# Kernel tuning notes

Measured on AMD Instinct MI355X. Metric: run time of the kernel, lower is better.

## Reference

```python
import jax, jax.numpy as jnp
import numpy as np


def setup_inputs() -> dict:
    key = jax.random.key(0)
    kq, kk, kv = jax.random.split(key, 3)
    B, H, S, D = 2, 16, 2048, 64
    Q = jax.random.normal(kq, (B, H, S, D), dtype=jnp.float32)
    K = jax.random.normal(kk, (B, H, S, D), dtype=jnp.float32)
    V = jax.random.normal(kv, (B, H, S, D), dtype=jnp.float32)
    # causal mask: 1 = keep, 0 = masked (masked_fill on mask == 0)
    mask = jnp.tril(jnp.ones((S, S), dtype=bool))[None, None, :, :]
    return {"V": V, "Q": Q, "K": K, "Fk": D, "mask": mask}


def reference(V, Q, K, Fk, mask):
    scale = 1.0 / jnp.sqrt(jnp.asarray(Fk, dtype=jnp.float32))
    # [B,H,S,S] scores
    C = jnp.einsum("bhqd,bhkd->bhqk", Q, K) * scale
    C = jnp.where(mask, C, jnp.asarray(-1e9, dtype=C.dtype))
    C = jax.nn.softmax(C, axis=-1)
    return jnp.einsum("bhqk,bhkd->bhqd", C, V)
```

## Files before the change

### kernel.cpp

```cpp
#include <hip/hip_runtime.h>
#include <hip/hip_bf16.h>

typedef __bf16 bf16x8 __attribute__((ext_vector_type(8)));
typedef __bf16 bf16x4 __attribute__((ext_vector_type(4)));
typedef __bf16 bf16x2 __attribute__((ext_vector_type(2)));
typedef float f32x4 __attribute__((ext_vector_type(4)));
typedef float f32x16 __attribute__((ext_vector_type(16)));

#define S_LEN 2048
#define D_DIM 64
#define NQT   32

static __device__ __forceinline__ unsigned pk2(float a, float b) {
  bf16x2 t; t[0] = (__bf16)a; t[1] = (__bf16)b;
  return __builtin_bit_cast(unsigned, t);
}

__global__ __launch_bounds__(256) void preprocess_kernel(
    const float* __restrict__ Kg, const float* __restrict__ Vg,
    unsigned char* __restrict__ Kb, unsigned char* __restrict__ Vt) {
  __shared__ float buf[2048];
  const int tid  = threadIdx.x;
  const int tile = blockIdx.x;
  const float* kg = Kg + (long)tile * 2048;
  const float* vg = Vg + (long)tile * 2048;
  unsigned char* kb = Kb + (long)tile * 4096;
  unsigned char* vt = Vt + (long)tile * 4096;

  const int l = tid & 63, f = tid >> 6, h = l >> 5;

  {
    const float* kr = kg + (l & 31) * 64 + f * 16 + h * 8;
    float4 a = *reinterpret_cast<const float4*>(kr);
    float4 b = *reinterpret_cast<const float4*>(kr + 4);
    bf16x8 t;
    t[0]=(__bf16)a.x; t[1]=(__bf16)a.y; t[2]=(__bf16)a.z; t[3]=(__bf16)a.w;
    t[4]=(__bf16)b.x; t[5]=(__bf16)b.y; t[6]=(__bf16)b.z; t[7]=(__bf16)b.w;
    *reinterpret_cast<bf16x8*>(kb + tid * 16) = t;
  }
  #pragma unroll
  for (int i = 0; i < 2; ++i) {
    int idx = tid + 256 * i;
    *reinterpret_cast<float4*>(buf + idx * 4) =
        *reinterpret_cast<const float4*>(vg + idx * 4);
  }
  __syncthreads();
  {
    int dt = f >> 1, ks = f & 1;
    int d  = dt * 32 + (l & 31);
    int k0 = ks * 16 + h * 8;
    bf16x8 t;
    #pragma unroll
    for (int j = 0; j < 8; ++j) t[j] = (__bf16)buf[(k0 + j) * 64 + d];
    *reinterpret_cast<bf16x8*>(vt + tid * 16) = t;
  }
}

__global__ __launch_bounds__(128, 4) void attn_fwd_w32s(
    const float* __restrict__ Qg, const unsigned char* __restrict__ Kb,
    const unsigned char* __restrict__ Vt, float* __restrict__ Og) {
  __shared__ float o_sm[2][32][68];
  __shared__ float m_sm[2][32];
  __shared__ float l_sm[2][32];

  const int tid  = threadIdx.x;
  const int lane = tid & 63;
  const int w    = tid >> 6;
  const int qc   = lane & 31;
  const int h    = lane >> 5;

  const int lb = blockIdx.x;
  const int e  = lb & 7;
  const int s  = lb >> 3;
  const int bh = e + 8 * (s >> 6);
  const int qg = 63 - (s & 63);
  const long base = (long)bh * (S_LEN * D_DIM);
  const int q0 = qg * 32;
  const int NT = qg + 1;

  bf16x8 qf[4];
  {
    const float qsc = 0.125f * 1.44269504f;
    const float* qp = Qg + base + (long)(q0 + qc) * D_DIM + h * 8;
    #pragma unroll
    for (int t = 0; t < 4; ++t) {
      float4 f0 = *reinterpret_cast<const float4*>(qp + t * 16);
      float4 f1 = *reinterpret_cast<const float4*>(qp + t * 16 + 4);
      bf16x8 q;
      q[0]=(__bf16)(f0.x*qsc); q[1]=(__bf16)(f0.y*qsc);
      q[2]=(__bf16)(f0.z*qsc); q[3]=(__bf16)(f0.w*qsc);
      q[4]=(__bf16)(f1.x*qsc); q[5]=(__bf16)(f1.y*qsc);
      q[6]=(__bf16)(f1.z*qsc); q[7]=(__bf16)(f1.w*qsc);
      qf[t] = q;
    }
  }

  f32x16 po0, po1;
  #pragma unroll
  for (int r = 0; r < 16; ++r) { po0[r] = 0.f; po1[r] = 0.f; }
  float m_run = -1e30f, l_run = 0.f;

  const unsigned char* kb_bh = Kb + (long)bh * 64 * 4096 + lane * 16;
  const unsigned char* vt_bh = Vt + (long)bh * 64 * 4096 + lane * 16;

  bf16x8 kfr[4], vfr[4];
  auto ldK = [&](int kt) {
    const unsigned char* p = kb_bh + (long)kt * 4096;
    #pragma unroll
    for (int t = 0; t < 4; ++t)
      kfr[t] = *reinterpret_cast<const bf16x8*>(p + t * 1024);
  };
  auto ldV = [&](int kt) {
    const unsigned char* p = vt_bh + (long)kt * 4096;
    #pragma unroll
    for (int t = 0; t < 4; ++t)
      vfr[t] = *reinterpret_cast<const bf16x8*>(p + t * 1024);
  };

  ldK(w);
  ldV(w);

  for (int kt = w; kt < NT; kt += 2) {
    const bool more = (kt + 2 < NT);

    f32x16 sa;
    #pragma unroll
    for (int r = 0; r < 16; ++r) sa[r] = 0.f;
    __builtin_amdgcn_s_setprio(1);
    #pragma unroll
    for (int t = 0; t < 4; ++t)
      sa = __builtin_amdgcn_mfma_f32_32x32x16_bf16(kfr[t], qf[t], sa, 0, 0, 0);
    __builtin_amdgcn_s_setprio(0);

    if (more) ldK(kt + 2);

    if (kt == NT - 1) {
      #pragma unroll
      for (int r = 0; r < 16; ++r)
        if (((r & 3) + 8 * (r >> 2) + 4 * h) > qc) sa[r] = -1e30f;
    }

    float rmax;
    {
      float a0 = fmaxf(fmaxf(sa[0], sa[1]),  fmaxf(sa[2], sa[3]));
      float a1 = fmaxf(fmaxf(sa[4], sa[5]),  fmaxf(sa[6], sa[7]));
      float a2 = fmaxf(fmaxf(sa[8], sa[9]),  fmaxf(sa[10], sa[11]));
      float a3 = fmaxf(fmaxf(sa[12], sa[13]), fmaxf(sa[14], sa[15]));
      rmax = fmaxf(fmaxf(a0, a1), fmaxf(a2, a3));
      rmax = fmaxf(rmax, __shfl_xor(rmax, 32));
    }

    if (__any(rmax > m_run + 8.0f)) {
      float mn    = fmaxf(m_run, rmax);
      float alpha = exp2f(m_run - mn);
      m_run = mn;
      l_run *= alpha;
      #pragma unroll
      for (int r = 0; r < 16; ++r) {
        float ar = __shfl(alpha, (r & 3) + 8 * (r >> 2) + 4 * h);
        po0[r] *= ar;
        po1[r] *= ar;
      }
    }

    #pragma unroll
    for (int r = 0; r < 16; ++r) sa[r] = exp2f(sa[r] - m_run);
    {
      float s0 = (sa[0] + sa[1]) + (sa[2] + sa[3]);
      float s1 = (sa[4] + sa[5]) + (sa[6] + sa[7]);
      float s2 = (sa[8] + sa[9]) + (sa[10] + sa[11]);
      float s3 = (sa[12] + sa[13]) + (sa[14] + sa[15]);
      float rs = (s0 + s1) + (s2 + s3);
      l_run += rs + __shfl_xor(rs, 32);
    }

    bf16x8 pa0, pa1;
    {
      unsigned k0 = pk2(sa[0], sa[1]),   k1 = pk2(sa[2], sa[3]);
      unsigned k2 = pk2(sa[4], sa[5]),   k3 = pk2(sa[6], sa[7]);
      unsigned k4 = pk2(sa[8], sa[9]),   k5 = pk2(sa[10], sa[11]);
      unsigned k6 = pk2(sa[12], sa[13]), k7 = pk2(sa[14], sa[15]);
      unsigned x02 = h ? k0 : k2, x13 = h ? k1 : k3;
      unsigned x46 = h ? k4 : k6, x57 = h ? k5 : k7;
      unsigned p02 = (unsigned)__shfl_xor((int)x02, 32);
      unsigned p13 = (unsigned)__shfl_xor((int)x13, 32);
      unsigned p46 = (unsigned)__shfl_xor((int)x46, 32);
      unsigned p57 = (unsigned)__shfl_xor((int)x57, 32);
      union { unsigned u[4]; bf16x8 v; } a, b;
      a.u[0] = h ? p02 : k0;  a.u[1] = h ? p13 : k1;
      a.u[2] = h ? k2 : p02;  a.u[3] = h ? k3 : p13;
      b.u[0] = h ? p46 : k4;  b.u[1] = h ? p57 : k5;
      b.u[2] = h ? k6 : p46;  b.u[3] = h ? k7 : p57;
      pa0 = a.v;
      pa1 = b.v;
    }

    __builtin_amdgcn_s_setprio(1);
    po0 = __builtin_amdgcn_mfma_f32_32x32x16_bf16(pa0, vfr[0], po0, 0, 0, 0);
    po0 = __builtin_amdgcn_mfma_f32_32x32x16_bf16(pa1, vfr[1], po0, 0, 0, 0);
    po1 = __builtin_amdgcn_mfma_f32_32x32x16_bf16(pa0, vfr[2], po1, 0, 0, 0);
    po1 = __builtin_amdgcn_mfma_f32_32x32x16_bf16(pa1, vfr[3], po1, 0, 0, 0);
    __builtin_amdgcn_s_setprio(0);

    if (more) ldV(kt + 2);
  }

  #pragma unroll
  for (int r = 0; r < 16; ++r) {
    int crow = (r & 3) + 8 * (r >> 2) + 4 * h;
    o_sm[w][crow][qc]      = po0[r];
    o_sm[w][crow][qc + 32] = po1[r];
  }
  if (h == 0) { m_sm[w][qc] = m_run; l_sm[w][qc] = l_run; }
  __syncthreads();

  {
    const int q  = tid >> 2;
    const int d0 = (tid & 3) * 16;
    float m0 = m_sm[0][q], m1 = m_sm[1][q];
    float M  = fmaxf(m0, m1);
    float a0 = exp2f(m0 - M), a1 = exp2f(m1 - M);
    float inv = 1.0f / (a0 * l_sm[0][q] + a1 * l_sm[1][q]);
    const float* r0 = &o_sm[0][q][d0];
    const float* r1 = &o_sm[1][q][d0];
    float* og = Og + base + (long)(q0 + q) * D_DIM + d0;
    #pragma unroll
    for (int i = 0; i < 4; ++i) {
      float4 x0 = *reinterpret_cast<const float4*>(r0 + 4 * i);
      float4 x1 = *reinterpret_cast<const float4*>(r1 + 4 * i);
      float4 o;
      o.x = (a0 * x0.x + a1 * x1.x) * inv;
      o.y = (a0 * x0.y + a1 * x1.y) * inv;
      o.z = (a0 * x0.z + a1 * x1.z) * inv;
      o.w = (a0 * x0.w + a1 * x1.w) * inv;
      *reinterpret_cast<float4*>(og + 4 * i) = o;
    }
  }
}

__global__ __launch_bounds__(256) void attn_fwd_fallback(
    const float* __restrict__ Vg, const float* __restrict__ Qg,
    const float* __restrict__ Kg, float* __restrict__ Og) {
  __shared__ __align__(16) unsigned char k_lds[64 * 128];
  __shared__ __align__(16) unsigned char vt_lds[64 * 128];
  __shared__ __align__(16) unsigned char p_lds[4][16 * 128];

  const int tid  = threadIdx.x;
  const int lane = tid & 63;
  const int w    = tid >> 6;
  const int lr   = lane & 15;
  const int lg   = lane >> 4;
  const int swz  = (lr & 7) << 4;

  const int lb = blockIdx.x;
  const int e  = lb & 7;
  const int s  = lb >> 3;
  const int bh = e + 8 * (s >> 5);
  const int qs = s & 31;
  const int qt = (qs & 1) ? (NQT - 1 - (qs >> 1)) : (qs >> 1);
  const long base = (long)bh * (S_LEN * D_DIM);
  const int q0 = qt * 64;

  bf16x8 qf[2];
  {
    const float qsc = 0.125f * 1.44269504f;
    const float* qp = Qg + base + (q0 + w * 16 + lr) * D_DIM + lg * 8;
    #pragma unroll
    for (int c = 0; c < 2; ++c) {
      float4 f0 = *reinterpret_cast<const float4*>(qp + c * 32);
      float4 f1 = *reinterpret_cast<const float4*>(qp + c * 32 + 4);
      bf16x8 t;
      t[0]=(__bf16)(f0.x*qsc); t[1]=(__bf16)(f0.y*qsc);
      t[2]=(__bf16)(f0.z*qsc); t[3]=(__bf16)(f0.w*qsc);
      t[4]=(__bf16)(f1.x*qsc); t[5]=(__bf16)(f1.y*qsc);
      t[6]=(__bf16)(f1.z*qsc); t[7]=(__bf16)(f1.w*qsc);
      qf[c] = t;
    }
  }
  bf16x8 onesf;
  #pragma unroll
  for (int j = 0; j < 8; ++j) onesf[j] = (lr == 0) ? (__bf16)1.0f : (__bf16)0.0f;

  f32x4 po[4], pl;
  float m_run = -1e30f;
  #pragma unroll
  for (int j = 0; j < 4; ++j) po[j] = (f32x4){0.f,0.f,0.f,0.f};
  pl = (f32x4){0.f,0.f,0.f,0.f};

  float4 kreg[4];
  float  vreg[16];
  const int d_ = lane;
  const int kb = w;

  auto load_regs = [&](int kt) {
    const float* kg = Kg + base + kt * (64 * D_DIM);
    #pragma unroll
    for (int i = 0; i < 4; ++i) {
      int idx = tid + 256 * i;
      int r = idx >> 4, f4 = idx & 15;
      kreg[i] = *reinterpret_cast<const float4*>(kg + r * 64 + f4 * 4);
    }
    const float* vg = Vg + base + kt * (64 * D_DIM);
    #pragma unroll
    for (int j = 0; j < 8; ++j) {
      vreg[j]     = vg[(kb * 8 + j) * 64 + d_];
      vreg[8 + j] = vg[((kb + 4) * 8 + j) * 64 + d_];
    }
  };
  auto write_buf = [&]() {
    #pragma unroll
    for (int i = 0; i < 4; ++i) {
      int idx = tid + 256 * i;
      int r = idx >> 4, f4 = idx & 15;
      bf16x4 t;
      t[0]=(__bf16)kreg[i].x; t[1]=(__bf16)kreg[i].y;
      t[2]=(__bf16)kreg[i].z; t[3]=(__bf16)kreg[i].w;
      int b = r * 128 + ((f4 * 8) ^ ((r & 7) << 4));
      *reinterpret_cast<bf16x4*>(&k_lds[b]) = t;
    }
    bf16x8 t0, t1;
    #pragma unroll
    for (int j = 0; j < 8; ++j) { t0[j] = (__bf16)vreg[j]; t1[j] = (__bf16)vreg[8+j]; }
    int b0 = d_ * 128 + ((kb * 16) ^ ((d_ & 7) << 4));
    int b1 = d_ * 128 + (((kb + 4) * 16) ^ ((d_ & 7) << 4));
    *reinterpret_cast<bf16x8*>(&vt_lds[b0]) = t0;
    *reinterpret_cast<bf16x8*>(&vt_lds[b1]) = t1;
  };

  load_regs(0);
  write_buf();
  __syncthreads();

  for (int kt = 0; kt <= qt; ++kt) {
    const bool last = (kt == qt);
    if (!last) load_regs(kt + 1);

    f32x4 sa[4];
    #pragma unroll
    for (int ct = 0; ct < 4; ++ct) sa[ct] = (f32x4){0.f,0.f,0.f,0.f};
    #pragma unroll
    for (int ct = 0; ct < 4; ++ct) {
      #pragma unroll
      for (int c = 0; c < 2; ++c) {
        int b = (ct * 16 + lr) * 128 + ((lg * 16 + c * 64) ^ swz);
        bf16x8 kf = *reinterpret_cast<const bf16x8*>(&k_lds[b]);
        sa[ct] = __builtin_amdgcn_mfma_f32_16x16x32_bf16(kf, qf[c], sa[ct], 0, 0, 0);
      }
    }
    if (last) {
      #pragma unroll
      for (int ct = 0; ct < 4; ++ct)
        #pragma unroll
        for (int j = 0; j < 4; ++j)
          if (ct * 16 + lg * 4 + j > w * 16 + lr) sa[ct][j] = -1e30f;
    }
    float rmax = sa[0][0];
    #pragma unroll
    for (int ct = 0; ct < 4; ++ct)
      #pragma unroll
      for (int j = 0; j < 4; ++j) rmax = fmaxf(rmax, sa[ct][j]);
    rmax = fmaxf(rmax, __shfl_xor(rmax, 16));
    rmax = fmaxf(rmax, __shfl_xor(rmax, 32));
    float mn    = fmaxf(m_run, rmax);
    float alpha = exp2f(m_run - mn);
    m_run = mn;
    #pragma unroll
    for (int ct = 0; ct < 4; ++ct) {
      bf16x4 t;
      #pragma unroll
      for (int j = 0; j < 4; ++j) t[j] = (__bf16)exp2f(sa[ct][j] - mn);
      int b = lr * 128 + ((ct * 32 + lg * 8) ^ swz);
      *reinterpret_cast<bf16x4*>(&p_lds[w][b]) = t;
    }
    float aj[4];
    #pragma unroll
    for (int j = 0; j < 4; ++j) aj[j] = __shfl(alpha, (lane & 48) | (lg * 4 + j));
    #pragma unroll
    for (int j = 0; j < 4; ++j) {
      pl[j] *= aj[j];
      #pragma unroll
      for (int dt = 0; dt < 4; ++dt) po[dt][j] *= aj[j];
    }
    #pragma unroll
    for (int c = 0; c < 2; ++c) {
      int ab = lr * 128 + ((lg * 16 + c * 64) ^ swz);
      bf16x8 pa = *reinterpret_cast<const bf16x8*>(&p_lds[w][ab]);
      pl = __builtin_amdgcn_mfma_f32_16x16x32_bf16(pa, onesf, pl, 0, 0, 0);
      #pragma unroll
      for (int dt = 0; dt < 4; ++dt) {
        int vb_ = (dt * 16 + lr) * 128 + ((lg * 16 + c * 64) ^ swz);
        bf16x8 vb = *reinterpret_cast<const bf16x8*>(&vt_lds[vb_]);
        po[dt] = __builtin_amdgcn_mfma_f32_16x16x32_bf16(pa, vb, po[dt], 0, 0, 0);
      }
    }
    if (!last) {
      __syncthreads();
      write_buf();
      __syncthreads();
    }
  }
  #pragma unroll
  for (int j = 0; j < 4; ++j) {
    float lv  = __shfl(pl[j], lane & 48);
    float inv = 1.0f / lv;
    int row = q0 + w * 16 + lg * 4 + j;
    #pragma unroll
    for (int dt = 0; dt < 4; ++dt)
      Og[base + row * D_DIM + dt * 16 + lr] = po[dt][j] * inv;
  }
}

extern "C" void kernel_launch(void* const* d_in, const int* in_sizes, int n_in,
                              void* d_out, int out_size, void* d_ws, size_t ws_size,
                              hipStream_t stream) {
  const float* V = (const float*)d_in[0];
  const float* Q = (const float*)d_in[1];
  const float* K = (const float*)d_in[2];
  float* O = (float*)d_out;
  const size_t need = (size_t)2 * 32 * 64 * 4096;
  if (ws_size >= need) {
    unsigned char* Kb = (unsigned char*)d_ws;
    unsigned char* Vt = Kb + (size_t)32 * 64 * 4096;
    preprocess_kernel<<<dim3(2048), dim3(256), 0, stream>>>(K, V, Kb, Vt);
    attn_fwd_w32s<<<dim3(2048), dim3(128), 0, stream>>>(Q, Kb, Vt, O);
  } else {
    attn_fwd_fallback<<<dim3(1024), dim3(256), 0, stream>>>(V, Q, K, O);
  }
}
```

Measured before the change: 62.42 us.

## Pair causal query tiles per block and split KV across four waves

Each block now processes two 32-row query tiles in sequence, a long one (63-pi) and a short one (pi), so every block does the same amount of causal work. The block grows from two to four waves, which split the KV tiles with stride 4 and merge their partial softmax results through LDS. The grid is halved to 1024 blocks. This removes the tail caused by unequal causal tile lengths, at the cost of a sequential dependency between the two phases and more LDS per block, which may lower occupancy.

```diff
diff --git a/kernel.cpp b/kernel.cpp
--- a/kernel.cpp
+++ b/kernel.cpp
@@ -56,12 +56,12 @@
   }
 }
 
-__global__ __launch_bounds__(128, 4) void attn_fwd_w32s(
+__global__ __launch_bounds__(256, 4) void attn_fwd_pair(
     const float* __restrict__ Qg, const unsigned char* __restrict__ Kb,
     const unsigned char* __restrict__ Vt, float* __restrict__ Og) {
-  __shared__ float o_sm[2][32][68];
-  __shared__ float m_sm[2][32];
-  __shared__ float l_sm[2][32];
+  __shared__ float o_sm[4][32][68];
+  __shared__ float m_sm[4][32];
+  __shared__ float l_sm[4][32];
 
   const int tid  = threadIdx.x;
   const int lane = tid & 63;
@@ -72,33 +72,9 @@
   const int lb = blockIdx.x;
   const int e  = lb & 7;
   const int s  = lb >> 3;
-  const int bh = e + 8 * (s >> 6);
-  const int qg = 63 - (s & 63);
+  const int bh = e + 8 * (s >> 5);
+  const int pi = s & 31;
   const long base = (long)bh * (S_LEN * D_DIM);
-  const int q0 = qg * 32;
-  const int NT = qg + 1;
-
-  bf16x8 qf[4];
-  {
-    const float qsc = 0.125f * 1.44269504f;
-    const float* qp = Qg + base + (long)(q0 + qc) * D_DIM + h * 8;
-    #pragma unroll
-    for (int t = 0; t < 4; ++t) {
-      float4 f0 = *reinterpret_cast<const float4*>(qp + t * 16);
-      float4 f1 = *reinterpret_cast<const float4*>(qp + t * 16 + 4);
-      bf16x8 q;
-      q[0]=(__bf16)(f0.x*qsc); q[1]=(__bf16)(f0.y*qsc);
-      q[2]=(__bf16)(f0.z*qsc); q[3]=(__bf16)(f0.w*qsc);
-      q[4]=(__bf16)(f1.x*qsc); q[5]=(__bf16)(f1.y*qsc);
-      q[6]=(__bf16)(f1.z*qsc); q[7]=(__bf16)(f1.w*qsc);
-      qf[t] = q;
-    }
-  }
-
-  f32x16 po0, po1;
-  #pragma unroll
-  for (int r = 0; r < 16; ++r) { po0[r] = 0.f; po1[r] = 0.f; }
-  float m_run = -1e30f, l_run = 0.f;
 
   const unsigned char* kb_bh = Kb + (long)bh * 64 * 4096 + lane * 16;
   const unsigned char* vt_bh = Vt + (long)bh * 64 * 4096 + lane * 16;
@@ -117,123 +93,156 @@
       vfr[t] = *reinterpret_cast<const bf16x8*>(p + t * 1024);
   };
 
-  ldK(w);
-  ldV(w);
-
-  for (int kt = w; kt < NT; kt += 2) {
-    const bool more = (kt + 2 < NT);
-
-    f32x16 sa;
-    #pragma unroll
-    for (int r = 0; r < 16; ++r) sa[r] = 0.f;
-    __builtin_amdgcn_s_setprio(1);
-    #pragma unroll
-    for (int t = 0; t < 4; ++t)
-      sa = __builtin_amdgcn_mfma_f32_32x32x16_bf16(kfr[t], qf[t], sa, 0, 0, 0);
-    __builtin_amdgcn_s_setprio(0);
-
-    if (more) ldK(kt + 2);
-
-    if (kt == NT - 1) {
-      #pragma unroll
-      for (int r = 0; r < 16; ++r)
-        if (((r & 3) + 8 * (r >> 2) + 4 * h) > qc) sa[r] = -1e30f;
-    }
-
-    float rmax;
+  #pragma unroll
+  for (int phase = 0; phase < 2; ++phase) {
+    const int qg = phase ? pi : (63 - pi);
+    const int q0 = qg * 32;
+    const int NT = qg + 1;
+
+    bf16x8 qf[4];
     {
-      float a0 = fmaxf(fmaxf(sa[0], sa[1]),  fmaxf(sa[2], sa[3]));
-      float a1 = fmaxf(fmaxf(sa[4], sa[5]),  fmaxf(sa[6], sa[7]));
-      float a2 = fmaxf(fmaxf(sa[8], sa[9]),  fmaxf(sa[10], sa[11]));
-      float a3 = fmaxf(fmaxf(sa[12], sa[13]), fmaxf(sa[14], sa[15]));
-      rmax = fmaxf(fmaxf(a0, a1), fmaxf(a2, a3));
-      rmax = fmaxf(rmax, __shfl_xor(rmax, 32));
-    }
-
-    if (__any(rmax > m_run + 8.0f)) {
-      float mn    = fmaxf(m_run, rmax);
-      float alpha = exp2f(m_run - mn);
-      m_run = mn;
-      l_run *= alpha;
-      #pragma unroll
-      for (int r = 0; r < 16; ++r) {
-        float ar = __shfl(alpha, (r & 3) + 8 * (r >> 2) + 4 * h);
-        po0[r] *= ar;
-        po1[r] *= ar;
-      }
-    }
-
-    #pragma unroll
-    for (int r = 0; r < 16; ++r) sa[r] = exp2f(sa[r] - m_run);
+      const float qsc = 0.125f * 1.44269504f;
+      const float* qp = Qg + base + (long)(q0 + qc) * D_DIM + h * 8;
+      #pragma unroll
+      for (int t = 0; t < 4; ++t) {
+        float4 f0 = *reinterpret_cast<const float4*>(qp + t * 16);
+        float4 f1 = *reinterpret_cast<const float4*>(qp + t * 16 + 4);
+        bf16x8 q;
+        q[0]=(__bf16)(f0.x*qsc); q[1]=(__bf16)(f0.y*qsc);
+        q[2]=(__bf16)(f0.z*qsc); q[3]=(__bf16)(f0.w*qsc);
+        q[4]=(__bf16)(f1.x*qsc); q[5]=(__bf16)(f1.y*qsc);
+        q[6]=(__bf16)(f1.z*qsc); q[7]=(__bf16)(f1.w*qsc);
+        qf[t] = q;
+      }
+    }
+
+    f32x16 po0, po1;
+    #pragma unroll
+    for (int r = 0; r < 16; ++r) { po0[r] = 0.f; po1[r] = 0.f; }
+    float m_run = -1e30f, l_run = 0.f;
+
+    ldK(w);
+    ldV(w);
+
+    for (int kt = w; kt < NT; kt += 4) {
+      const bool more = (kt + 4 < NT);
+
+      f32x16 sa;
+      #pragma unroll
+      for (int r = 0; r < 16; ++r) sa[r] = 0.f;
+      __builtin_amdgcn_s_setprio(1);
+      #pragma unroll
+      for (int t = 0; t < 4; ++t)
+        sa = __builtin_amdgcn_mfma_f32_32x32x16_bf16(kfr[t], qf[t], sa, 0, 0, 0);
+      __builtin_amdgcn_s_setprio(0);
+
+      if (more) ldK(kt + 4);
+
+      if (kt == NT - 1) {
+        #pragma unroll
+        for (int r = 0; r < 16; ++r)
+          if (((r & 3) + 8 * (r >> 2) + 4 * h) > qc) sa[r] = -1e30f;
+      }
+
+      float rmax;
+      {
+        float a0 = fmaxf(fmaxf(sa[0], sa[1]),  fmaxf(sa[2], sa[3]));
+        float a1 = fmaxf(fmaxf(sa[4], sa[5]),  fmaxf(sa[6], sa[7]));
+        float a2 = fmaxf(fmaxf(sa[8], sa[9]),  fmaxf(sa[10], sa[11]));
+        float a3 = fmaxf(fmaxf(sa[12], sa[13]), fmaxf(sa[14], sa[15]));
+        rmax = fmaxf(fmaxf(a0, a1), fmaxf(a2, a3));
+        rmax = fmaxf(rmax, __shfl_xor(rmax, 32));
+      }
+
+      if (__any(rmax > m_run + 8.0f)) {
+        float mn    = fmaxf(m_run, rmax);
+        float alpha = exp2f(m_run - mn);
+        m_run = mn;
+        l_run *= alpha;
+        #pragma unroll
+        for (int r = 0; r < 16; ++r) {
+          float ar = __shfl(alpha, (r & 3) + 8 * (r >> 2) + 4 * h);
+          po0[r] *= ar;
+          po1[r] *= ar;
+        }
+      }
+
+      #pragma unroll
+      for (int r = 0; r < 16; ++r) sa[r] = exp2f(sa[r] - m_run);
+      {
+        float s0 = (sa[0] + sa[1]) + (sa[2] + sa[3]);
+        float s1 = (sa[4] + sa[5]) + (sa[6] + sa[7]);
+        float s2 = (sa[8] + sa[9]) + (sa[10] + sa[11]);
+        float s3 = (sa[12] + sa[13]) + (sa[14] + sa[15]);
+        float rs = (s0 + s1) + (s2 + s3);
+        l_run += rs + __shfl_xor(rs, 32);
+      }
+
+      bf16x8 pa0, pa1;
+      {
+        unsigned k0 = pk2(sa[0], sa[1]),   k1 = pk2(sa[2], sa[3]);
+        unsigned k2 = pk2(sa[4], sa[5]),   k3 = pk2(sa[6], sa[7]);
+        unsigned k4 = pk2(sa[8], sa[9]),   k5 = pk2(sa[10], sa[11]);
+        unsigned k6 = pk2(sa[12], sa[13]), k7 = pk2(sa[14], sa[15]);
+        unsigned x02 = h ? k0 : k2, x13 = h ? k1 : k3;
+        unsigned x46 = h ? k4 : k6, x57 = h ? k5 : k7;
+        unsigned p02 = (unsigned)__shfl_xor((int)x02, 32);
+        unsigned p13 = (unsigned)__shfl_xor((int)x13, 32);
+        unsigned p46 = (unsigned)__shfl_xor((int)x46, 32);
+        unsigned p57 = (unsigned)__shfl_xor((int)x57, 32);
+        union { unsigned u[4]; bf16x8 v; } a, b;
+        a.u[0] = h ? p02 : k0;  a.u[1] = h ? p13 : k1;
+        a.u[2] = h ? k2 : p02;  a.u[3] = h ? k3 : p13;
+        b.u[0] = h ? p46 : k4;  b.u[1] = h ? p57 : k5;
+        b.u[2] = h ? k6 : p46;  b.u[3] = h ? k7 : p57;
+        pa0 = a.v;
+        pa1 = b.v;
+      }
+
+      __builtin_amdgcn_s_setprio(1);
+      po0 = __builtin_amdgcn_mfma_f32_32x32x16_bf16(pa0, vfr[0], po0, 0, 0, 0);
+      po0 = __builtin_amdgcn_mfma_f32_32x32x16_bf16(pa1, vfr[1], po0, 0, 0, 0);
+      po1 = __builtin_amdgcn_mfma_f32_32x32x16_bf16(pa0, vfr[2], po1, 0, 0, 0);
+      po1 = __builtin_amdgcn_mfma_f32_32x32x16_bf16(pa1, vfr[3], po1, 0, 0, 0);
+      __builtin_amdgcn_s_setprio(0);
+
+      if (more) ldV(kt + 4);
+    }
+
+    if (phase) __syncthreads();
+    #pragma unroll
+    for (int r = 0; r < 16; ++r) {
+      int crow = (r & 3) + 8 * (r >> 2) + 4 * h;
+      o_sm[w][crow][qc]      = po0[r];
+      o_sm[w][crow][qc + 32] = po1[r];
+    }
+    if (h == 0) { m_sm[w][qc] = m_run; l_sm[w][qc] = l_run; }
+    __syncthreads();
+
     {
-      float s0 = (sa[0] + sa[1]) + (sa[2] + sa[3]);
-      float s1 = (sa[4] + sa[5]) + (sa[6] + sa[7]);
-      float s2 = (sa[8] + sa[9]) + (sa[10] + sa[11]);
-      float s3 = (sa[12] + sa[13]) + (sa[14] + sa[15]);
-      float rs = (s0 + s1) + (s2 + s3);
-      l_run += rs + __shfl_xor(rs, 32);
-    }
-
-    bf16x8 pa0, pa1;
-    {
-      unsigned k0 = pk2(sa[0], sa[1]),   k1 = pk2(sa[2], sa[3]);
-      unsigned k2 = pk2(sa[4], sa[5]),   k3 = pk2(sa[6], sa[7]);
-      unsigned k4 = pk2(sa[8], sa[9]),   k5 = pk2(sa[10], sa[11]);
-      unsigned k6 = pk2(sa[12], sa[13]), k7 = pk2(sa[14], sa[15]);
-      unsigned x02 = h ? k0 : k2, x13 = h ? k1 : k3;
-      unsigned x46 = h ? k4 : k6, x57 = h ? k5 : k7;
-      unsigned p02 = (unsigned)__shfl_xor((int)x02, 32);
-      unsigned p13 = (unsigned)__shfl_xor((int)x13, 32);
-      unsigned p46 = (unsigned)__shfl_xor((int)x46, 32);
-      unsigned p57 = (unsigned)__shfl_xor((int)x57, 32);
-      union { unsigned u[4]; bf16x8 v; } a, b;
-      a.u[0] = h ? p02 : k0;  a.u[1] = h ? p13 : k1;
-      a.u[2] = h ? k2 : p02;  a.u[3] = h ? k3 : p13;
-      b.u[0] = h ? p46 : k4;  b.u[1] = h ? p57 : k5;
-      b.u[2] = h ? k6 : p46;  b.u[3] = h ? k7 : p57;
-      pa0 = a.v;
-      pa1 = b.v;
-    }
-
-    __builtin_amdgcn_s_setprio(1);
-    po0 = __builtin_amdgcn_mfma_f32_32x32x16_bf16(pa0, vfr[0], po0, 0, 0, 0);
-    po0 = __builtin_amdgcn_mfma_f32_32x32x16_bf16(pa1, vfr[1], po0, 0, 0, 0);
-    po1 = __builtin_amdgcn_mfma_f32_32x32x16_bf16(pa0, vfr[2], po1, 0, 0, 0);
-    po1 = __builtin_amdgcn_mfma_f32_32x32x16_bf16(pa1, vfr[3], po1, 0, 0, 0);
-    __builtin_amdgcn_s_setprio(0);
-
-    if (more) ldV(kt + 2);
-  }
-
-  #pragma unroll
-  for (int r = 0; r < 16; ++r) {
-    int crow = (r & 3) + 8 * (r >> 2) + 4 * h;
-    o_sm[w][crow][qc]      = po0[r];
-    o_sm[w][crow][qc + 32] = po1[r];
-  }
-  if (h == 0) { m_sm[w][qc] = m_run; l_sm[w][qc] = l_run; }
-  __syncthreads();
-
-  {
-    const int q  = tid >> 2;
-    const int d0 = (tid & 3) * 16;
-    float m0 = m_sm[0][q], m1 = m_sm[1][q];
-    float M  = fmaxf(m0, m1);
-    float a0 = exp2f(m0 - M), a1 = exp2f(m1 - M);
-    float inv = 1.0f / (a0 * l_sm[0][q] + a1 * l_sm[1][q]);
-    const float* r0 = &o_sm[0][q][d0];
-    const float* r1 = &o_sm[1][q][d0];
-    float* og = Og + base + (long)(q0 + q) * D_DIM + d0;
-    #pragma unroll
-    for (int i = 0; i < 4; ++i) {
-      float4 x0 = *reinterpret_cast<const float4*>(r0 + 4 * i);
-      float4 x1 = *reinterpret_cast<const float4*>(r1 + 4 * i);
-      float4 o;
-      o.x = (a0 * x0.x + a1 * x1.x) * inv;
-      o.y = (a0 * x0.y + a1 * x1.y) * inv;
-      o.z = (a0 * x0.z + a1 * x1.z) * inv;
-      o.w = (a0 * x0.w + a1 * x1.w) * inv;
-      *reinterpret_cast<float4*>(og + 4 * i) = o;
+      const int q  = tid >> 3;
+      const int d0 = (tid & 7) * 8;
+      float m0 = m_sm[0][q], m1 = m_sm[1][q];
+      float m2 = m_sm[2][q], m3 = m_sm[3][q];
+      float M  = fmaxf(fmaxf(m0, m1), fmaxf(m2, m3));
+      float a0 = exp2f(m0 - M), a1 = exp2f(m1 - M);
+      float a2 = exp2f(m2 - M), a3 = exp2f(m3 - M);
+      float inv = 1.0f / (a0 * l_sm[0][q] + a1 * l_sm[1][q]
+                        + a2 * l_sm[2][q] + a3 * l_sm[3][q]);
+      float* og = Og + base + (long)(q0 + q) * D_DIM + d0;
+      #pragma unroll
+      for (int half = 0; half < 2; ++half) {
+        float4 x0 = *reinterpret_cast<const float4*>(&o_sm[0][q][d0 + 4 * half]);
+        float4 x1 = *reinterpret_cast<const float4*>(&o_sm[1][q][d0 + 4 * half]);
+        float4 x2 = *reinterpret_cast<const float4*>(&o_sm[2][q][d0 + 4 * half]);
+        float4 x3 = *reinterpret_cast<const float4*>(&o_sm[3][q][d0 + 4 * half]);
+        float4 o;
+        o.x = (a0 * x0.x + a1 * x1.x + a2 * x2.x + a3 * x3.x) * inv;
+        o.y = (a0 * x0.y + a1 * x1.y + a2 * x2.y + a3 * x3.y) * inv;
+        o.z = (a0 * x0.z + a1 * x1.z + a2 * x2.z + a3 * x3.z) * inv;
+        o.w = (a0 * x0.w + a1 * x1.w + a2 * x2.w + a3 * x3.w) * inv;
+        *reinterpret_cast<float4*>(og + 4 * half) = o;
+      }
     }
   }
 }
@@ -422,7 +431,7 @@
     unsigned char* Kb = (unsigned char*)d_ws;
     unsigned char* Vt = Kb + (size_t)32 * 64 * 4096;
     preprocess_kernel<<<dim3(2048), dim3(256), 0, stream>>>(K, V, Kb, Vt);
-    attn_fwd_w32s<<<dim3(2048), dim3(128), 0, stream>>>(Q, Kb, Vt, O);
+    attn_fwd_pair<<<dim3(1024), dim3(256), 0, stream>>>(Q, Kb, Vt, O);
   } else {
     attn_fwd_fallback<<<dim3(1024), dim3(256), 0, stream>>>(V, Q, K, O);
   }
```

Result: no change. 61.91 us (-0.8%).
